# Optimization experiments

Hardware: AMD Instinct MI355X
Metric: run time of the kernel (lower is better)

## Reference

```python
import jax, jax.numpy as jnp
import numpy as np


def setup_inputs() -> dict:
    key = jax.random.key(0)
    ks = jax.random.split(key, 5)
    T, B, C, H, K = 2048, 8, 1024, 16, 7
    s = 1.0 / np.sqrt(C)
    return {
        "x": jax.random.normal(ks[0], (T, B, C), dtype=jnp.float32),
        "w_weight": jax.random.normal(ks[1], (H * K, C), dtype=jnp.float32) * s,
        "glu_w": jax.random.normal(ks[2], (2 * H, C), dtype=jnp.float32) * s,
        "glu_b": jnp.zeros((2 * H,), dtype=jnp.float32),
        "out_w": jax.random.normal(ks[3], (C, C), dtype=jnp.float32) * s,
        "out_b": jnp.zeros((C,), dtype=jnp.float32),
        "padding_l": 6,
    }


def reference(x, w_weight, glu_w, glu_b, out_w, out_b, padding_l):
    # x: (T, B, C) in TBC format
    T, B, C = x.shape
    H = glu_w.shape[0] // 2
    K = w_weight.shape[0] // H
    R = C // H  # channels per head

    # GLU gate: C -> 2H, split last dim, a * sigmoid(b)  -> (T, B, H)
    g = (x @ glu_w.T + glu_b).reshape(T, B, H, 2)
    gate = g[..., 0] * jax.nn.sigmoid(g[..., 1])

    # per-position per-head kernel weights, softmax over K -> (T, B, H, K)
    w = jax.nn.softmax((x @ w_weight.T).reshape(T, B, H, K), axis=-1)

    # depthwise dynamic conv: out[t] = sum_k w[t,k] * x_pad[t + k]
    xh = x.reshape(T, B, H, R)
    xp = jnp.pad(xh, ((padding_l, K - 1 - padding_l), (0, 0), (0, 0), (0, 0)))
    conv = jnp.zeros_like(xh)
    for k in range(K):  # K is small & static; avoids (B,H,T,K,R) unfold blowup
        conv = conv + w[..., k:k + 1] * jax.lax.dynamic_slice_in_dim(xp, k, T, axis=0)

    # gate per head, merge heads, output projection
    out = (conv * gate[..., None]).reshape(T, B, C)
    return out @ out_w.T + out_b
```

## Files before the change

### kernel.cpp

```cpp
#include <hip/hip_runtime.h>
#include <hip/hip_bf16.h>
#include <stdint.h>

#define T_DIM 2048
#define B_DIM 8
#define C_DIM 1024
#define H_DIM 16
#define K_DIM 7
#define M_DIM (T_DIM * B_DIM)
#define NLOG 144
#define CW_STRIDE 128
#define LSM_STRIDE 146

typedef __attribute__((ext_vector_type(8))) short short8;
typedef __attribute__((ext_vector_type(4))) float floatx4;

__device__ __forceinline__ ushort f2bf(float f) {
    __hip_bfloat16 h = __float2bfloat16(f);
    return *(ushort*)&h;
}

#define S_W  ((size_t)112 * C_DIM)
#define S_G  ((size_t)32 * C_DIM)
#define S_O  ((size_t)C_DIM * C_DIM)
#define S_WG (S_W + S_G)
#define S_CVT (S_WG + S_O)

__global__ __launch_bounds__(256) void cvt_w_kernel(
    const float* __restrict__ w_weight, const float* __restrict__ glu_w,
    const float* __restrict__ out_w,
    ushort* __restrict__ wb, ushort* __restrict__ Wb)
{
    size_t gid = ((size_t)blockIdx.x * 256 + threadIdx.x) * 4;
    const float* src; ushort* dst; size_t off;
    if (gid < S_W)            { src = w_weight; dst = wb;       off = gid; }
    else if (gid < S_WG)      { src = glu_w;    dst = wb + S_W; off = gid - S_W; }
    else                      { src = out_w;    dst = Wb;       off = gid - S_WG; }
    float4 v = *(const float4*)(src + off);
    ushort4 o; o.x = f2bf(v.x); o.y = f2bf(v.y); o.z = f2bf(v.z); o.w = f2bf(v.w);
    *(ushort4*)(dst + off) = o;
}

__global__ __launch_bounds__(512) void logits_kernel(
    const float* __restrict__ x,
    const ushort* __restrict__ wb,
    const float* __restrict__ glu_b,
    float* __restrict__ cw)
{
    __shared__ float lsm[64][LSM_STRIDE];

    const int tid = threadIdx.x;
    const int wave = tid >> 6, lane = tid & 63;
    const int g = wave & 3;
    const int kh = wave >> 2;
    const int fr = lane & 15, q = lane >> 4;
    const int m0 = blockIdx.x * 64;
    const int mrow = m0 + g * 16 + fr;
    const int kb = kh * 512;

    floatx4 acc[9];
#pragma unroll
    for (int j = 0; j < 9; ++j) acc[j] = (floatx4){0.f, 0.f, 0.f, 0.f};

    const float* arow = x + (size_t)mrow * C_DIM + kb + q * 8;
    const ushort* brow = wb + (size_t)fr * C_DIM + kb + q * 8;

    float4 a0 = *(const float4*)(arow);
    float4 a1 = *(const float4*)(arow + 4);

#pragma unroll 2
    for (int kc = 0; kc < 16; ++kc) {
        short8 a;
        a[0] = (short)f2bf(a0.x); a[1] = (short)f2bf(a0.y);
        a[2] = (short)f2bf(a0.z); a[3] = (short)f2bf(a0.w);
        a[4] = (short)f2bf(a1.x); a[5] = (short)f2bf(a1.y);
        a[6] = (short)f2bf(a1.z); a[7] = (short)f2bf(a1.w);
        if (kc < 15) {
            a0 = *(const float4*)(arow + (kc + 1) * 32);
            a1 = *(const float4*)(arow + (kc + 1) * 32 + 4);
        }
#pragma unroll
        for (int j = 0; j < 9; ++j) {
            short8 b = *(const short8*)(brow + (size_t)j * 16 * C_DIM + kc * 32);
            acc[j] = __builtin_amdgcn_mfma_f32_16x16x32_bf16(a, b, acc[j], 0, 0, 0);
        }
    }

    if (kh == 0) {
#pragma unroll
        for (int j = 0; j < 9; ++j)
#pragma unroll
            for (int r = 0; r < 4; ++r)
                lsm[g * 16 + q * 4 + r][j * 16 + fr] = acc[j][r];
    }
    __syncthreads();
    if (kh == 1) {
#pragma unroll
        for (int j = 0; j < 9; ++j)
#pragma unroll
            for (int r = 0; r < 4; ++r)
                lsm[g * 16 + q * 4 + r][j * 16 + fr] += acc[j][r];
    }
    __syncthreads();

    {
        const int row = tid >> 3;
        const int hbase = (tid & 7) * 2;
        float* crow = cw + (size_t)(m0 + row) * CW_STRIDE;
#pragma unroll
        for (int hh = 0; hh < 2; ++hh) {
            const int h = hbase + hh;
            float l[K_DIM];
            float mx = -1e30f;
#pragma unroll
            for (int k = 0; k < K_DIM; ++k) { l[k] = lsm[row][h * K_DIM + k]; mx = fmaxf(mx, l[k]); }
            float s = 0.f;
#pragma unroll
            for (int k = 0; k < K_DIM; ++k) { l[k] = __expf(l[k] - mx); s += l[k]; }
            float inv = 1.f / s;
#pragma unroll
            for (int k = 0; k < K_DIM; ++k) crow[h * K_DIM + k] = l[k] * inv;
            float ga = lsm[row][112 + 2 * h] + glu_b[2 * h];
            float gb = lsm[row][113 + 2 * h] + glu_b[2 * h + 1];
            crow[112 + h] = ga * (1.f / (1.f + __expf(-gb)));
        }
    }
}

__global__ __launch_bounds__(256) void conv_kernel(
    const float* __restrict__ x,
    const float* __restrict__ cw,
    const int* __restrict__ padding_l_,
    ushort* __restrict__ y)
{
    const int lb = (blockIdx.x & 7) * 512 + (blockIdx.x >> 3);
    const int wave = threadIdx.x >> 6, lane = threadIdx.x & 63;
    const int m = lb * 4 + wave;
    const int t = m >> 3;
    const int pad = *padding_l_;
    const int h = lane >> 2;

    const float* crow = cw + (size_t)m * CW_STRIDE;
    float wt[K_DIM];
#pragma unroll
    for (int k = 0; k < K_DIM; ++k) wt[k] = crow[h * K_DIM + k];
    const float g = crow[112 + h];

    const int c0 = lane * 16;
    float av[16];
#pragma unroll
    for (int i = 0; i < 16; ++i) av[i] = 0.f;

#pragma unroll
    for (int k = 0; k < K_DIM; ++k) {
        int ts = t + k - pad;
        if (ts < 0 || ts >= T_DIM) continue;
        float wv = wt[k];
        const float4* xp = (const float4*)(x + ((size_t)m + 8 * (k - pad)) * C_DIM + c0);
        float4 u0 = xp[0], u1 = xp[1], u2 = xp[2], u3 = xp[3];
        av[0]  += wv * u0.x; av[1]  += wv * u0.y; av[2]  += wv * u0.z; av[3]  += wv * u0.w;
        av[4]  += wv * u1.x; av[5]  += wv * u1.y; av[6]  += wv * u1.z; av[7]  += wv * u1.w;
        av[8]  += wv * u2.x; av[9]  += wv * u2.y; av[10] += wv * u2.z; av[11] += wv * u2.w;
        av[12] += wv * u3.x; av[13] += wv * u3.y; av[14] += wv * u3.z; av[15] += wv * u3.w;
    }

    uint32_t o[8];
#pragma unroll
    for (int i = 0; i < 8; ++i)
        o[i] = (uint32_t)f2bf(av[2 * i] * g) | ((uint32_t)f2bf(av[2 * i + 1] * g) << 16);
    uint4* yr = (uint4*)(y + (size_t)m * C_DIM + c0);
    yr[0] = (uint4){o[0], o[1], o[2], o[3]};
    yr[1] = (uint4){o[4], o[5], o[6], o[7]};
}

__global__ __launch_bounds__(512, 2) void out_gemm(
    const ushort* __restrict__ y,
    const ushort* __restrict__ Wb,
    const float* __restrict__ bias,
    float* __restrict__ out)
{
    __shared__ __align__(16) ushort SM[2][4][128 * 64];

    const int orig = (blockIdx.x & 7) * 32 + (blockIdx.x >> 3);
    const int bm = orig >> 2;
    const int bn = orig & 3;
    const int m0 = bm * 256, n0 = bn * 256;
    const int tid = threadIdx.x;
    const int lane = tid & 63, wave = tid >> 6;
    const int wr = wave >> 2;
    const int wc = wave & 3;
    const int fr = lane & 15, q = lane >> 4;
    const int g0 = ((q) ^ (fr & 7)) * 8;
    const int g1 = ((4 + q) ^ (fr & 7)) * 8;

    floatx4 acc[8][4];
#pragma unroll
    for (int i = 0; i < 8; ++i)
#pragma unroll
        for (int j = 0; j < 4; ++j) acc[i][j] = (floatx4){0.f, 0.f, 0.f, 0.f};

    auto stageH = [&](int buf, int mat, int half, int k0) {
        const ushort* src = mat ? Wb : y;
        const int row0 = (mat ? n0 : m0) + half * 128;
        ushort* dst = &SM[buf][mat * 2 + half][0];
#pragma unroll
        for (int j = 0; j < 2; ++j) {
            int idx = j * 512 + tid;
            int r = idx >> 3, gl = idx & 7;
            int gs = gl ^ (r & 7);
            __builtin_amdgcn_global_load_lds(
                (const __attribute__((address_space(1))) void*)(src + (size_t)(row0 + r) * C_DIM + k0 + gs * 8),
                (__attribute__((address_space(3))) void*)(dst + idx * 8), 16, 0, 0);
        }
    };

    stageH(0, 0, 0, 0);  stageH(0, 0, 1, 0);
    stageH(0, 1, 0, 0);  stageH(0, 1, 1, 0);
    stageH(1, 1, 0, 64); stageH(1, 1, 1, 64);
    asm volatile("s_waitcnt vmcnt(4)" ::: "memory");
    __builtin_amdgcn_s_barrier();
    asm volatile("" ::: "memory");

    short8 a[4][2], b[4][2];
    for (int t = 0; t < 16; ++t) {
        const int buf = t & 1;
        const ushort* Ar = &SM[buf][wr][0];
        const ushort* Br = &SM[buf][2 + (wc >> 1)][0];
        const int brb = (wc & 1) * 64;

#pragma unroll
        for (int mf = 0; mf < 4; ++mf) {
            int ro = (mf * 16 + fr) * 64;
            a[mf][0] = *(const short8*)(Ar + ro + g0);
            a[mf][1] = *(const short8*)(Ar + ro + g1);
        }
#pragma unroll
        for (int nf = 0; nf < 2; ++nf) {
            int ro = (brb + nf * 16 + fr) * 64;
            b[nf][0] = *(const short8*)(Br + ro + g0);
            b[nf][1] = *(const short8*)(Br + ro + g1);
        }
        if (t + 1 < 16) stageH(buf ^ 1, 0, 0, (t + 1) * 64);
        __builtin_amdgcn_s_barrier();
        asm volatile("s_waitcnt lgkmcnt(0)" ::: "memory");
        __builtin_amdgcn_s_setprio(1);
#pragma unroll
        for (int ks = 0; ks < 2; ++ks)
#pragma unroll
            for (int mf = 0; mf < 4; ++mf)
#pragma unroll
                for (int nf = 0; nf < 2; ++nf)
                    acc[mf][nf] = __builtin_amdgcn_mfma_f32_16x16x32_bf16(a[mf][ks], b[nf][ks], acc[mf][nf], 0, 0, 0);
        __builtin_amdgcn_s_setprio(0);
        asm volatile("" ::: "memory");
        __builtin_amdgcn_s_barrier();
        asm volatile("" ::: "memory");

#pragma unroll
        for (int nf = 2; nf < 4; ++nf) {
            int ro = (brb + nf * 16 + fr) * 64;
            b[nf][0] = *(const short8*)(Br + ro + g0);
            b[nf][1] = *(const short8*)(Br + ro + g1);
        }
        if (t + 1 < 16) stageH(buf ^ 1, 0, 1, (t + 1) * 64);
        __builtin_amdgcn_s_barrier();
        asm volatile("s_waitcnt lgkmcnt(0)" ::: "memory");
        __builtin_amdgcn_s_setprio(1);
#pragma unroll
        for (int ks = 0; ks < 2; ++ks)
#pragma unroll
            for (int mf = 0; mf < 4; ++mf)
#pragma unroll
                for (int nf = 2; nf < 4; ++nf)
                    acc[mf][nf] = __builtin_amdgcn_mfma_f32_16x16x32_bf16(a[mf][ks], b[nf][ks], acc[mf][nf], 0, 0, 0);
        __builtin_amdgcn_s_setprio(0);
        asm volatile("" ::: "memory");
        __builtin_amdgcn_s_barrier();
        asm volatile("" ::: "memory");

#pragma unroll
        for (int mf = 0; mf < 4; ++mf) {
            int ro = ((mf + 4) * 16 + fr) * 64;
            a[mf][0] = *(const short8*)(Ar + ro + g0);
            a[mf][1] = *(const short8*)(Ar + ro + g1);
        }
        if (t + 2 < 16) stageH(buf, 1, 0, (t + 2) * 64);
        __builtin_amdgcn_s_barrier();
        asm volatile("s_waitcnt lgkmcnt(0)" ::: "memory");
        __builtin_amdgcn_s_setprio(1);
#pragma unroll
        for (int ks = 0; ks < 2; ++ks)
#pragma unroll
            for (int mf = 0; mf < 4; ++mf)
#pragma unroll
                for (int nf = 0; nf < 2; ++nf)
                    acc[mf + 4][nf] = __builtin_amdgcn_mfma_f32_16x16x32_bf16(a[mf][ks], b[nf][ks], acc[mf + 4][nf], 0, 0, 0);
        __builtin_amdgcn_s_setprio(0);
        asm volatile("" ::: "memory");
        __builtin_amdgcn_s_barrier();
        asm volatile("" ::: "memory");

        if (t + 2 < 16) stageH(buf, 1, 1, (t + 2) * 64);
        if (t < 14)       { asm volatile("s_waitcnt vmcnt(4)" ::: "memory"); }
        else if (t == 14) { asm volatile("s_waitcnt vmcnt(0)" ::: "memory"); }
        __builtin_amdgcn_s_barrier();
        asm volatile("" ::: "memory");
        __builtin_amdgcn_s_setprio(1);
#pragma unroll
        for (int ks = 0; ks < 2; ++ks)
#pragma unroll
            for (int mf = 0; mf < 4; ++mf)
#pragma unroll
                for (int nf = 2; nf < 4; ++nf)
                    acc[mf + 4][nf] = __builtin_amdgcn_mfma_f32_16x16x32_bf16(a[mf][ks], b[nf][ks], acc[mf + 4][nf], 0, 0, 0);
        __builtin_amdgcn_s_setprio(0);
        asm volatile("" ::: "memory");
        __builtin_amdgcn_s_barrier();
        asm volatile("" ::: "memory");
    }

#pragma unroll
    for (int nf = 0; nf < 4; ++nf) {
        int n = n0 + wc * 64 + nf * 16 + fr;
        float bv = bias[n];
#pragma unroll
        for (int mf = 0; mf < 8; ++mf) {
#pragma unroll
            for (int r = 0; r < 4; ++r) {
                int m = m0 + wr * 128 + mf * 16 + q * 4 + r;
                out[(size_t)m * C_DIM + n] = acc[mf][nf][r] + bv;
            }
        }
    }
}

extern "C" void kernel_launch(void* const* d_in, const int* in_sizes, int n_in,
                              void* d_out, int out_size, void* d_ws, size_t ws_size,
                              hipStream_t stream) {
    const float* x        = (const float*)d_in[0];
    const float* w_weight = (const float*)d_in[1];
    const float* glu_w    = (const float*)d_in[2];
    const float* glu_b    = (const float*)d_in[3];
    const float* out_w    = (const float*)d_in[4];
    const float* out_b    = (const float*)d_in[5];
    const int* padding_l  = (const int*)d_in[6];
    float* out = (float*)d_out;

    char* ws = (char*)d_ws;
    ushort* y  = (ushort*)ws;
    ushort* wb = y + (size_t)M_DIM * C_DIM;
    ushort* Wb = wb + S_WG;
    float* cwp = (float*)(Wb + S_O);

    cvt_w_kernel<<<S_CVT / 4 / 256, 256, 0, stream>>>(w_weight, glu_w, out_w, wb, Wb);
    logits_kernel<<<M_DIM / 64, 512, 0, stream>>>(x, wb, glu_b, cwp);
    conv_kernel<<<M_DIM / 4, 256, 0, stream>>>(x, cwp, padding_l, y);
    out_gemm<<<(M_DIM / 256) * (C_DIM / 256), 512, 0, stream>>>(y, Wb, out_b, out);
}
```

Measured before the change: 218.3 us.

## Fuse logits/softmax/gate computation with depthwise dynamic conv kernel

Merges the logits+softmax kernel and the conv kernel into one, keeping the softmax weights and gates in shared memory instead of writing them to a global buffer and reading them back. Each block now does the conv for its own 64 rows right after computing their weights, and block indices are remapped so neighbouring blocks share time-neighbour rows of x in cache. This removes one launch and the cw round trip, and lets x rows just read for the GEMM be reused from cache. The cost is extra shared memory, another barrier, and fewer blocks doing the conv part, which may lower parallelism for that phase.

Measured after the change: 210.6 us. -3.6%, faster.

```diff
diff --git a/kernel.cpp b/kernel.cpp
--- a/kernel.cpp
+++ b/kernel.cpp
@@ -9,7 +9,6 @@
 #define K_DIM 7
 #define M_DIM (T_DIM * B_DIM)
 #define NLOG 144
-#define CW_STRIDE 128
 #define LSM_STRIDE 146
 
 typedef __attribute__((ext_vector_type(8))) short short8;
@@ -41,20 +40,23 @@
     *(ushort4*)(dst + off) = o;
 }
 
-__global__ __launch_bounds__(512) void logits_kernel(
+__global__ __launch_bounds__(512) void logits_conv_kernel(
     const float* __restrict__ x,
     const ushort* __restrict__ wb,
     const float* __restrict__ glu_b,
-    float* __restrict__ cw)
+    const int* __restrict__ padding_l_,
+    ushort* __restrict__ y)
 {
     __shared__ float lsm[64][LSM_STRIDE];
+    __shared__ float gat[64][H_DIM];
 
     const int tid = threadIdx.x;
     const int wave = tid >> 6, lane = tid & 63;
     const int g = wave & 3;
     const int kh = wave >> 2;
     const int fr = lane & 15, q = lane >> 4;
-    const int m0 = blockIdx.x * 64;
+    const int orig = (blockIdx.x & 7) * 32 + (blockIdx.x >> 3);
+    const int m0 = orig * 64;
     const int mrow = m0 + g * 16 + fr;
     const int kb = kh * 512;
 
@@ -106,7 +108,6 @@
     {
         const int row = tid >> 3;
         const int hbase = (tid & 7) * 2;
-        float* crow = cw + (size_t)(m0 + row) * CW_STRIDE;
 #pragma unroll
         for (int hh = 0; hh < 2; ++hh) {
             const int h = hbase + hh;
@@ -119,58 +120,55 @@
             for (int k = 0; k < K_DIM; ++k) { l[k] = __expf(l[k] - mx); s += l[k]; }
             float inv = 1.f / s;
 #pragma unroll
-            for (int k = 0; k < K_DIM; ++k) crow[h * K_DIM + k] = l[k] * inv;
+            for (int k = 0; k < K_DIM; ++k) lsm[row][h * K_DIM + k] = l[k] * inv;
             float ga = lsm[row][112 + 2 * h] + glu_b[2 * h];
             float gb = lsm[row][113 + 2 * h] + glu_b[2 * h + 1];
-            crow[112 + h] = ga * (1.f / (1.f + __expf(-gb)));
-        }
-    }
-}
-
-__global__ __launch_bounds__(256) void conv_kernel(
-    const float* __restrict__ x,
-    const float* __restrict__ cw,
-    const int* __restrict__ padding_l_,
-    ushort* __restrict__ y)
-{
-    const int lb = (blockIdx.x & 7) * 512 + (blockIdx.x >> 3);
-    const int wave = threadIdx.x >> 6, lane = threadIdx.x & 63;
-    const int m = lb * 4 + wave;
-    const int t = m >> 3;
-    const int pad = *padding_l_;
-    const int h = lane >> 2;
-
-    const float* crow = cw + (size_t)m * CW_STRIDE;
-    float wt[K_DIM];
-#pragma unroll
-    for (int k = 0; k < K_DIM; ++k) wt[k] = crow[h * K_DIM + k];
-    const float g = crow[112 + h];
-
-    const int c0 = lane * 16;
-    float av[16];
-#pragma unroll
-    for (int i = 0; i < 16; ++i) av[i] = 0.f;
-
-#pragma unroll
-    for (int k = 0; k < K_DIM; ++k) {
-        int ts = t + k - pad;
-        if (ts < 0 || ts >= T_DIM) continue;
-        float wv = wt[k];
-        const float4* xp = (const float4*)(x + ((size_t)m + 8 * (k - pad)) * C_DIM + c0);
-        float4 u0 = xp[0], u1 = xp[1], u2 = xp[2], u3 = xp[3];
-        av[0]  += wv * u0.x; av[1]  += wv * u0.y; av[2]  += wv * u0.z; av[3]  += wv * u0.w;
-        av[4]  += wv * u1.x; av[5]  += wv * u1.y; av[6]  += wv * u1.z; av[7]  += wv * u1.w;
-        av[8]  += wv * u2.x; av[9]  += wv * u2.y; av[10] += wv * u2.z; av[11] += wv * u2.w;
-        av[12] += wv * u3.x; av[13] += wv * u3.y; av[14] += wv * u3.z; av[15] += wv * u3.w;
-    }
-
-    uint32_t o[8];
-#pragma unroll
-    for (int i = 0; i < 8; ++i)
-        o[i] = (uint32_t)f2bf(av[2 * i] * g) | ((uint32_t)f2bf(av[2 * i + 1] * g) << 16);
-    uint4* yr = (uint4*)(y + (size_t)m * C_DIM + c0);
-    yr[0] = (uint4){o[0], o[1], o[2], o[3]};
-    yr[1] = (uint4){o[4], o[5], o[6], o[7]};
+            gat[row][h] = ga * (1.f / (1.f + __expf(-gb)));
+        }
+    }
+    __syncthreads();
+
+    {
+        const int pad = *padding_l_;
+        const int h = lane >> 2;
+        const int c0 = lane * 16;
+#pragma unroll
+        for (int rr = 0; rr < 8; ++rr) {
+            const int r = wave * 8 + rr;
+            const int m = m0 + r;
+            const int t = m >> 3;
+
+            float wt[K_DIM];
+#pragma unroll
+            for (int k = 0; k < K_DIM; ++k) wt[k] = lsm[r][h * K_DIM + k];
+            const float gv = gat[r][h];
+
+            float av[16];
+#pragma unroll
+            for (int i = 0; i < 16; ++i) av[i] = 0.f;
+
+#pragma unroll
+            for (int k = 0; k < K_DIM; ++k) {
+                int ts = t + k - pad;
+                if (ts < 0 || ts >= T_DIM) continue;
+                float wv = wt[k];
+                const float4* xp = (const float4*)(x + ((size_t)m + 8 * (k - pad)) * C_DIM + c0);
+                float4 u0 = xp[0], u1 = xp[1], u2 = xp[2], u3 = xp[3];
+                av[0]  += wv * u0.x; av[1]  += wv * u0.y; av[2]  += wv * u0.z; av[3]  += wv * u0.w;
+                av[4]  += wv * u1.x; av[5]  += wv * u1.y; av[6]  += wv * u1.z; av[7]  += wv * u1.w;
+                av[8]  += wv * u2.x; av[9]  += wv * u2.y; av[10] += wv * u2.z; av[11] += wv * u2.w;
+                av[12] += wv * u3.x; av[13] += wv * u3.y; av[14] += wv * u3.z; av[15] += wv * u3.w;
+            }
+
+            uint32_t o[8];
+#pragma unroll
+            for (int i = 0; i < 8; ++i)
+                o[i] = (uint32_t)f2bf(av[2 * i] * gv) | ((uint32_t)f2bf(av[2 * i + 1] * gv) << 16);
+            uint4* yr = (uint4*)(y + (size_t)m * C_DIM + c0);
+            yr[0] = (uint4){o[0], o[1], o[2], o[3]};
+            yr[1] = (uint4){o[4], o[5], o[6], o[7]};
+        }
+    }
 }
 
 __global__ __launch_bounds__(512, 2) void out_gemm(
@@ -350,10 +348,8 @@
     ushort* y  = (ushort*)ws;
     ushort* wb = y + (size_t)M_DIM * C_DIM;
     ushort* Wb = wb + S_WG;
-    float* cwp = (float*)(Wb + S_O);
 
     cvt_w_kernel<<<S_CVT / 4 / 256, 256, 0, stream>>>(w_weight, glu_w, out_w, wb, Wb);
-    logits_kernel<<<M_DIM / 64, 512, 0, stream>>>(x, wb, glu_b, cwp);
-    conv_kernel<<<M_DIM / 4, 256, 0, stream>>>(x, cwp, padding_l, y);
+    logits_conv_kernel<<<M_DIM / 64, 512, 0, stream>>>(x, wb, glu_b, padding_l, y);
     out_gemm<<<(M_DIM / 256) * (C_DIM / 256), 512, 0, stream>>>(y, Wb, out_b, out);
 }
```
